# Performance work log

Hardware: AMD Instinct MI355X
Metric: run time of the kernel (lower is better)

The kernel has to match this reference:

```python
import jax, jax.numpy as jnp
import numpy as np

EPS = 1e-5
GROUPS = 32

def group_norm(x, w, b):
    B, C, D, H, W = x.shape
    g = x.reshape(B, GROUPS, C // GROUPS, D, H, W)
    mean = g.mean(axis=(2, 3, 4, 5), keepdims=True)
    var = g.var(axis=(2, 3, 4, 5), keepdims=True)
    g = (g - mean) * jax.lax.rsqrt(var + EPS)
    g = g.reshape(B, C, D, H, W)
    return g * w[None, :, None, None, None] + b[None, :, None, None, None]

def setup_inputs() -> dict:
    key = jax.random.key(0)
    ks = jax.random.split(key, 6)
    C = 256
    B, D, H, W = 2, 16, 16, 16
    xavier = math_scale = (6.0 / (C + C)) ** 0.5
    def xav(k):
        return jax.random.uniform(k, (C, C), jnp.float32, -xavier, xavier)
    return {
        "x": jax.random.normal(ks[0], (B, C, D, H, W), jnp.float32),
        "gn_w": jnp.ones((C,), jnp.float32),
        "gn_b": jnp.zeros((C,), jnp.float32),
        "wq": xav(ks[1]), "bq": jnp.zeros((C,), jnp.float32),
        "wk": xav(ks[2]), "bk": jnp.zeros((C,), jnp.float32),
        "wv": xav(ks[3]), "bv": jnp.zeros((C,), jnp.float32),
        "wp": xav(ks[4]), "bp": jnp.zeros((C,), jnp.float32),
    }

def reference(x, gn_w, gn_b, wq, bq, wk, bk, wv, bv, wp, bp):
    B, C, D, H, W = x.shape
    h = group_norm(x, gn_w, gn_b)
    hf = h.reshape(B, C, -1)  # (B, C, N)
    # 1x1x1 conv == channel-wise linear: weight (out_c, in_c)
    q = jnp.einsum('oc,bcn->bon', wq, hf) + bq[None, :, None]
    k = jnp.einsum('oc,bcn->bon', wk, hf) + bk[None, :, None]
    v = jnp.einsum('oc,bcn->bon', wv, hf) + bv[None, :, None]
    scale = C ** (-0.5)
    attn = jnp.einsum('bcn,bcm->bnm', q, k) * scale  # (B, N, N)
    attn = jax.nn.softmax(attn, axis=-1)
    out = jnp.einsum('bnm,bcm->bcn', attn, v)  # (B, C, N)
    out = jnp.einsum('oc,bcn->bon', wp, out) + bp[None, :, None]
    return x + out.reshape(B, C, D, H, W)
```

## Files before the change

### kernel.cpp

```cpp
#include <hip/hip_runtime.h>

#define C_DIM 256
#define N_SP  4096
#define B_DIM 2
#define CPG   8
#define EPS_GN 1e-5f
#define CN ((size_t)C_DIM * N_SP)

typedef unsigned short ushort_t;
typedef unsigned int uint_t;
typedef __attribute__((ext_vector_type(4))) float f32x4;
typedef __attribute__((ext_vector_type(16))) float f32x16;
typedef __attribute__((ext_vector_type(4))) unsigned int u32x4;
typedef __attribute__((ext_vector_type(8))) short bf16x8;

__device__ inline uint_t pkbf(float a, float b) {
  uint_t r;
  asm("v_cvt_pk_bf16_f32 %0, %1, %2" : "=v"(r) : "v"(a), "v"(b));
  return r;
}
__device__ inline float bf2f(uint_t u) {
  union { uint_t u; float f; } v; v.u = u << 16; return v.f;
}

#define GLOAD16(src, dst) __builtin_amdgcn_global_load_lds( \
    (const __attribute__((address_space(1))) unsigned int*)(src), \
    (__attribute__((address_space(3))) unsigned int*)(dst), 16, 0, 0)

__global__ __launch_bounds__(256) void wcvt_kernel(const float* __restrict__ wq,
    const float* __restrict__ wk, const float* __restrict__ wv,
    const float* __restrict__ wp, ushort_t* __restrict__ o) {
  int gid = blockIdx.x * 256 + threadIdx.x;
  int i4 = gid * 4;
  const float* s = (i4 < 65536) ? wq : (i4 < 131072) ? wk : (i4 < 196608) ? wv : wp;
  int off = i4 & 65535;
  float4 v = *(const float4*)(s + off);
  uint2 p; p.x = pkbf(v.x, v.y); p.y = pkbf(v.z, v.w);
  *(uint2*)&o[i4] = p;
}

__global__ __launch_bounds__(256) void gn_stats(const float* __restrict__ x,
    float* __restrict__ part) {
  const int bg = blockIdx.x, sub = blockIdx.y;
  const float* xp = x + (size_t)bg * CPG * N_SP + (size_t)sub * (CPG * N_SP / 4);
  const int tid = threadIdx.x;
  float s = 0.f, ss = 0.f;
  for (int i = tid; i < CPG * N_SP / 4; i += 256) {
    float v = xp[i];
    s += v; ss += v * v;
  }
#pragma unroll
  for (int off = 32; off > 0; off >>= 1) {
    s  += __shfl_down(s, off);
    ss += __shfl_down(ss, off);
  }
  __shared__ float rs[4], rss[4];
  const int wv = tid >> 6, ln = tid & 63;
  if (ln == 0) { rs[wv] = s; rss[wv] = ss; }
  __syncthreads();
  if (tid == 0) {
    part[(bg * 4 + sub) * 2]     = rs[0] + rs[1] + rs[2] + rs[3];
    part[(bg * 4 + sub) * 2 + 1] = rss[0] + rss[1] + rss[2] + rss[3];
  }
}

__global__ __launch_bounds__(256) void gn_apply(const float* __restrict__ x,
    const float* __restrict__ part, const float* __restrict__ w,
    const float* __restrict__ bgn, ushort_t* __restrict__ hT) {
  const int bg = blockIdx.x;
  const int b = bg >> 5, g = bg & 31;
  const int n0 = blockIdx.y * 256;
  const int tid = threadIdx.x;
  float S = 0.f, SS = 0.f;
#pragma unroll
  for (int i = 0; i < 4; ++i) {
    S  += part[(bg * 4 + i) * 2];
    SS += part[(bg * 4 + i) * 2 + 1];
  }
  const float mean = S / (float)(CPG * N_SP);
  const float var  = SS / (float)(CPG * N_SP) - mean * mean;
  const float rstd = rsqrtf(var + EPS_GN);
  float sc[8], sh[8];
#pragma unroll
  for (int c = 0; c < 8; ++c) {
    sc[c] = w[g * 8 + c] * rstd;
    sh[c] = bgn[g * 8 + c] - mean * sc[c];
  }
  __shared__ float tile[8][256];
  const float* xp = x + ((size_t)b * C_DIM + (size_t)g * CPG) * N_SP;
  for (int i = tid; i < 8 * 256; i += 256) {
    int cc = i >> 8, n = i & 255;
    tile[cc][n] = xp[(size_t)cc * N_SP + n0 + n];
  }
  __syncthreads();
  u32x4 pk4;
#pragma unroll
  for (int p = 0; p < 4; ++p)
    pk4[p] = pkbf(tile[2 * p][tid] * sc[2 * p] + sh[2 * p],
                  tile[2 * p + 1][tid] * sc[2 * p + 1] + sh[2 * p + 1]);
  *(u32x4*)&hT[((size_t)b * N_SP + n0 + tid) * C_DIM + g * 8] = pk4;
}

template <int MODE>
__global__ __launch_bounds__(256) void mgemm(
    const ushort_t* __restrict__ A, const ushort_t* __restrict__ Bm,
    const float* __restrict__ biasA, const float* __restrict__ biasB,
    ushort_t* __restrict__ outB, float* __restrict__ outF,
    const float* __restrict__ R, int aStride, int bStride, int ldo,
    size_t obStride) {
  __shared__ __align__(16) ushort_t a_lds[128 * 64];
  __shared__ __align__(16) ushort_t b_lds[128 * 64];
  const int bz = blockIdx.z;
  const ushort_t* Ab = A + (size_t)bz * aStride;
  const ushort_t* Bb = Bm + (size_t)bz * bStride;
  const int bm = blockIdx.y * 128, bn = blockIdx.x * 128;
  const int tid = threadIdx.x, wv = tid >> 6, ln = tid & 63;
  const int lo = ln & 15, g = ln >> 4;
  const int wr = wv >> 1, wc = wv & 1;

  f32x4 acc[4][4];
#pragma unroll
  for (int i = 0; i < 4; ++i)
#pragma unroll
    for (int j = 0; j < 4; ++j) acc[i][j] = (f32x4)(0.f);

  float bcol[4];
  float brow = 0.f;
  if (MODE == 0) {
#pragma unroll
    for (int ct = 0; ct < 4; ++ct) {
      int col = bn + wc * 64 + ct * 16 + lo;
      bcol[ct] = (col < 256) ? biasA[col] : biasB[col - 256];
    }
  } else {
    brow = biasA[bm + wr * 64 + ln];
  }

  for (int k0 = 0; k0 < C_DIM; k0 += 64) {
#pragma unroll
    for (int i = 0; i < 4; ++i) {
      int r0 = wv * 32 + i * 8;
      int row = r0 + (ln >> 3);
      GLOAD16(Ab + (size_t)(bm + row) * C_DIM + k0 + (((ln & 7) ^ (row & 7)) << 3),
              &a_lds[r0 * 64]);
      GLOAD16(Bb + (size_t)(bn + row) * C_DIM + k0 + (((ln & 7) ^ (row & 7)) << 3),
              &b_lds[r0 * 64]);
    }
    __syncthreads();
    bf16x8 af[4][2], bfr[4][2];
#pragma unroll
    for (int rt = 0; rt < 4; ++rt)
#pragma unroll
      for (int ks = 0; ks < 2; ++ks) {
        int row = wr * 64 + rt * 16 + lo;
        af[rt][ks] = *(const bf16x8*)&a_lds[row * 64 + (((ks * 4 + g) ^ (row & 7)) << 3)];
      }
#pragma unroll
    for (int ct = 0; ct < 4; ++ct)
#pragma unroll
      for (int ks = 0; ks < 2; ++ks) {
        int col = wc * 64 + ct * 16 + lo;
        bfr[ct][ks] = *(const bf16x8*)&b_lds[col * 64 + (((ks * 4 + g) ^ (col & 7)) << 3)];
      }
    __builtin_amdgcn_s_setprio(1);
#pragma unroll
    for (int ks = 0; ks < 2; ++ks)
#pragma unroll
      for (int rt = 0; rt < 4; ++rt)
#pragma unroll
        for (int ct = 0; ct < 4; ++ct)
          acc[rt][ct] = __builtin_amdgcn_mfma_f32_16x16x32_bf16(af[rt][ks], bfr[ct][ks], acc[rt][ct], 0, 0, 0);
    __builtin_amdgcn_s_setprio(0);
    __syncthreads();
  }

  float* wbase = (wv < 2 ? (float*)a_lds : (float*)b_lds) + (wv & 1) * 2048;
  const int grow = bm + wr * 64 + ln;
#pragma unroll
  for (int p = 0; p < 2; ++p) {
#pragma unroll
    for (int rt = 0; rt < 4; ++rt)
#pragma unroll
      for (int cth = 0; cth < 2; ++cth) {
        int ct = 2 * p + cth;
#pragma unroll
        for (int r = 0; r < 4; ++r) {
          int lrow = rt * 16 + 4 * g + r;
          int lcol = cth * 16 + lo;
          float v = acc[rt][ct][r];
          if (MODE == 0) v += bcol[ct];
          wbase[lrow * 32 + (lcol ^ ((lrow & 7) << 2))] = v;
        }
      }
    f32x4 buf[8];
#pragma unroll
    for (int cb = 0; cb < 8; ++cb) {
      int off = (4 * cb) ^ ((ln & 7) << 2);
      buf[cb] = *(const f32x4*)&wbase[ln * 32 + off];
    }
    const size_t obase = (size_t)grow * ldo + bn + wc * 64 + p * 32;
    if (MODE == 2) {
      const float* Rb = R + (size_t)bz * CN + obase;
      float* ob = outF + (size_t)bz * CN + obase;
#pragma unroll
      for (int cb = 0; cb < 8; ++cb) {
        f32x4 t = buf[cb];
        f32x4 rv = *(const f32x4*)&Rb[4 * cb];
#pragma unroll
        for (int j = 0; j < 4; ++j) t[j] += brow + rv[j];
        *(f32x4*)&ob[4 * cb] = t;
      }
    } else {
      float badd = (MODE == 0) ? 0.f : brow;
      ushort_t* ob = outB + (size_t)bz * obStride + obase;
      uint_t wpk[16];
#pragma unroll
      for (int k = 0; k < 16; ++k)
        wpk[k] = pkbf(buf[k >> 1][(k & 1) * 2] + badd, buf[k >> 1][(k & 1) * 2 + 1] + badd);
#pragma unroll
      for (int sidx = 0; sidx < 4; ++sidx) {
        u32x4 t;
        t[0] = wpk[4 * sidx]; t[1] = wpk[4 * sidx + 1];
        t[2] = wpk[4 * sidx + 2]; t[3] = wpk[4 * sidx + 3];
        *(u32x4*)&ob[sidx * 8] = t;
      }
    }
    __syncthreads();
  }
}

__device__ __forceinline__ void stage_kv(const ushort_t* __restrict__ ktb,
    const ushort_t* __restrict__ vtb, int k0, ushort_t* kbuf, ushort_t* vbuf,
    int wv, int ln) {
#pragma unroll
  for (int i = 0; i < 8; ++i) {
    int m = wv * 16 + i * 2 + (ln >> 5);
    int sl = ln & 31;
    GLOAD16(ktb + (size_t)(k0 + m) * 512 + ((sl ^ (m & 7)) * 8),
            kbuf + (wv * 16 + i * 2) * 256);
  }
#pragma unroll
  for (int i = 0; i < 8; ++i) {
    int c = wv * 64 + i * 8 + (ln >> 3);
    int sl = ln & 7;
    GLOAD16(vtb + (size_t)c * N_SP + k0 + ((sl ^ (c & 7)) * 8),
            vbuf + (wv * 64 + i * 8) * 64);
  }
}

__global__ __launch_bounds__(256, 1) void attn_mfma(
    const ushort_t* __restrict__ qk, const ushort_t* __restrict__ vt,
    ushort_t* __restrict__ pO, float* __restrict__ pml) {
  __shared__ __align__(16) ushort_t lds_all[32768 + 32768 + 9216];

  const int ksplit = blockIdx.y;
  const int b  = blockIdx.z;
  const int q0 = blockIdx.x * 128;
  const int tid = threadIdx.x;
  const int wv = tid >> 6;
  const int ln = tid & 63;
  const int lq = ln & 31;
  const int lh = ln >> 5;

  const ushort_t* qtb = qk + (size_t)b * N_SP * 512;
  const ushort_t* ktb = qtb + 256;
  const ushort_t* vtb = vt + (size_t)b * CN;
  ushort_t* p_base = lds_all + 65536 + wv * (32 * 72);

  bf16x8 qf[16];
  {
    const ushort_t* qp = qtb + (size_t)(q0 + wv * 32 + lq) * 512 + lh * 8;
#pragma unroll
    for (int ks = 0; ks < 16; ++ks) qf[ks] = *(const bf16x8*)(qp + ks * 16);
  }

  f32x16 oac[8];
#pragma unroll
  for (int i = 0; i < 8; ++i) oac[i] = (f32x16)(0.f);
  float m_run = -1e30f, l_run = 0.f;

  const int kbase = ksplit * 1024;
  stage_kv(ktb, vtb, kbase, lds_all, lds_all + 32768, wv, ln);
  __syncthreads();

  for (int t = 0; t < 16; ++t) {
    const int cur = t & 1;
    ushort_t* kb = lds_all + cur * 16384;
    ushort_t* vb = lds_all + 32768 + cur * 16384;
    if (t + 1 < 16)
      stage_kv(ktb, vtb, kbase + (t + 1) * 64,
               lds_all + (cur ^ 1) * 16384,
               lds_all + 32768 + (cur ^ 1) * 16384, wv, ln);

    f32x16 s0 = (f32x16)(0.f), s1 = (f32x16)(0.f);
    __builtin_amdgcn_s_setprio(1);
#pragma unroll
    for (int ks = 0; ks < 16; ++ks) {
      bf16x8 kf0 = *(const bf16x8*)&kb[(lq * 256 + ks * 16 + lh * 8) ^ ((lq & 7) << 3)];
      s0 = __builtin_amdgcn_mfma_f32_32x32x16_bf16(kf0, qf[ks], s0, 0, 0, 0);
      int m1 = 32 + lq;
      bf16x8 kf1 = *(const bf16x8*)&kb[(m1 * 256 + ks * 16 + lh * 8) ^ ((m1 & 7) << 3)];
      s1 = __builtin_amdgcn_mfma_f32_32x32x16_bf16(kf1, qf[ks], s1, 0, 0, 0);
    }
    __builtin_amdgcn_s_setprio(0);

    const float scale = 0.0625f;
    float mx[16];
#pragma unroll
    for (int r = 0; r < 16; ++r) mx[r] = fmaxf(s0[r], s1[r]);
#pragma unroll
    for (int r = 0; r < 8; ++r) mx[r] = fmaxf(mx[r], mx[r + 8]);
#pragma unroll
    for (int r = 0; r < 4; ++r) mx[r] = fmaxf(mx[r], mx[r + 4]);
    float pm = fmaxf(fmaxf(mx[0], mx[1]), fmaxf(mx[2], mx[3]));
    pm = fmaxf(pm, __shfl_xor(pm, 32));
    pm *= scale;
    float alpha = 1.f;
    if (!__all(pm <= m_run + 8.f)) {
      float mn = fmaxf(m_run, pm);
      alpha = __expf(m_run - mn);
      m_run = mn;
    }
    float rsum = 0.f;
#pragma unroll
    for (int g2 = 0; g2 < 4; ++g2) {
      float e00 = __expf(s0[4 * g2 + 0] * scale - m_run);
      float e01 = __expf(s0[4 * g2 + 1] * scale - m_run);
      float e02 = __expf(s0[4 * g2 + 2] * scale - m_run);
      float e03 = __expf(s0[4 * g2 + 3] * scale - m_run);
      float e10 = __expf(s1[4 * g2 + 0] * scale - m_run);
      float e11 = __expf(s1[4 * g2 + 1] * scale - m_run);
      float e12 = __expf(s1[4 * g2 + 2] * scale - m_run);
      float e13 = __expf(s1[4 * g2 + 3] * scale - m_run);
      rsum += ((e00 + e01) + (e02 + e03)) + ((e10 + e11) + (e12 + e13));
      uint2 wa; wa.x = pkbf(e00, e01); wa.y = pkbf(e02, e03);
      *(uint2*)&p_base[lq * 72 + 8 * g2 + 4 * lh] = wa;
      uint2 wb2; wb2.x = pkbf(e10, e11); wb2.y = pkbf(e12, e13);
      *(uint2*)&p_base[lq * 72 + 32 + 8 * g2 + 4 * lh] = wb2;
    }
    rsum += __shfl_xor(rsum, 32);
    l_run = l_run * alpha + rsum;
    if (!__all(alpha == 1.f)) {
#pragma unroll
      for (int i = 0; i < 8; ++i) oac[i] *= alpha;
    }

    __builtin_amdgcn_s_setprio(1);
#pragma unroll
    for (int ks2 = 0; ks2 < 4; ++ks2) {
      bf16x8 pf = *(const bf16x8*)&p_base[lq * 72 + ks2 * 16 + lh * 8];
#pragma unroll
      for (int ot = 0; ot < 8; ++ot) {
        int c = ot * 32 + lq;
        bf16x8 vf = *(const bf16x8*)&vb[(c * 64 + ks2 * 16 + lh * 8) ^ ((c & 7) << 3)];
        oac[ot] = __builtin_amdgcn_mfma_f32_32x32x16_bf16(vf, pf, oac[ot], 0, 0, 0);
      }
    }
    __builtin_amdgcn_s_setprio(0);
    __syncthreads();
  }

  float* sb = (float*)lds_all + wv * 8192;
#pragma unroll
  for (int ot = 0; ot < 8; ++ot)
#pragma unroll
    for (int r = 0; r < 16; ++r) {
      int cl = (r & 3) + 8 * (r >> 2) + 4 * lh;
      int c = ot * 32 + cl;
      sb[lq * 256 + (c ^ ((lq & 7) << 2))] = oac[ot][r];
    }
  {
    const int q = ln >> 1, half = ln & 1;
    const size_t row32 = (((size_t)(ksplit * B_DIM + b) * N_SP) + q0 + wv * 32 + q) * 128;
    uint_t* pO32 = (uint_t*)pO;
#pragma unroll
    for (int j = 0; j < 32; ++j) {
      f32x4 v4 = *(const f32x4*)&sb[q * 256 + ((half * 128 + 4 * j) ^ ((q & 7) << 2))];
      uint2 pk2; pk2.x = pkbf(v4[0], v4[1]); pk2.y = pkbf(v4[2], v4[3]);
      *(uint2*)&pO32[row32 + half * 64 + 2 * j] = pk2;
    }
  }
  if (ln < 32) {
    int qn = q0 + wv * 32 + lq;
    size_t mi = (((size_t)(ksplit * B_DIM + b) * N_SP) + qn) * 2;
    pml[mi] = m_run;
    pml[mi + 1] = l_run;
  }
}

__global__ __launch_bounds__(256) void merge_kernel(const ushort_t* __restrict__ pO,
    const float* __restrict__ pml, ushort_t* __restrict__ aoT) {
  const int b = blockIdx.y;
  const int n = blockIdx.x * 16 + (threadIdx.x >> 4);
  const int cg = threadIdx.x & 15;
  float mi[4], li[4];
#pragma unroll
  for (int i = 0; i < 4; ++i) {
    size_t o = (((size_t)(i * B_DIM + b) * N_SP) + n) * 2;
    mi[i] = pml[o]; li[i] = pml[o + 1];
  }
  float ms = fmaxf(fmaxf(mi[0], mi[1]), fmaxf(mi[2], mi[3]));
  float wsum = 0.f, wi[4];
#pragma unroll
  for (int i = 0; i < 4; ++i) { wi[i] = __expf(mi[i] - ms); wsum += wi[i] * li[i]; }
  float inv = 1.f / wsum;
  float acc[16] = {};
#pragma unroll
  for (int i = 0; i < 4; ++i) {
    const ushort_t* p = pO + (((size_t)(i * B_DIM + b) * N_SP) + n) * C_DIM + cg * 16;
    u32x4 a = *(const u32x4*)p;
    u32x4 c2 = *(const u32x4*)(p + 8);
#pragma unroll
    for (int j = 0; j < 4; ++j) {
      acc[2 * j]     += wi[i] * bf2f(a[j] & 0xffffu);
      acc[2 * j + 1] += wi[i] * bf2f(a[j] >> 16);
      acc[8 + 2 * j]     += wi[i] * bf2f(c2[j] & 0xffffu);
      acc[8 + 2 * j + 1] += wi[i] * bf2f(c2[j] >> 16);
    }
  }
  ushort_t* ob = aoT + ((size_t)b * N_SP + n) * C_DIM + cg * 16;
  u32x4 o0, o1;
#pragma unroll
  for (int k = 0; k < 4; ++k) o0[k] = pkbf(acc[2 * k] * inv, acc[2 * k + 1] * inv);
#pragma unroll
  for (int k = 0; k < 4; ++k) o1[k] = pkbf(acc[8 + 2 * k] * inv, acc[8 + 2 * k + 1] * inv);
  *(u32x4*)&ob[0] = o0;
  *(u32x4*)&ob[8] = o1;
}

extern "C" void kernel_launch(void* const* d_in, const int* in_sizes, int n_in,
                              void* d_out, int out_size, void* d_ws, size_t ws_size,
                              hipStream_t stream) {
  const float* x   = (const float*)d_in[0];
  const float* gnw = (const float*)d_in[1];
  const float* gnb = (const float*)d_in[2];
  const float* wq  = (const float*)d_in[3];
  const float* bq  = (const float*)d_in[4];
  const float* wk  = (const float*)d_in[5];
  const float* bk  = (const float*)d_in[6];
  const float* wv  = (const float*)d_in[7];
  const float* bv  = (const float*)d_in[8];
  const float* wp  = (const float*)d_in[9];
  const float* bp  = (const float*)d_in[10];
  float* out = (float*)d_out;

  char* w8 = (char*)d_ws;
  ushort_t* hT  = (ushort_t*)(w8);
  ushort_t* wb  = (ushort_t*)(w8 + (4u << 20));
  ushort_t* qkw = (ushort_t*)(w8 + (4u << 20) + (1u << 19));
  ushort_t* vN  = (ushort_t*)(w8 + (12u << 20) + (1u << 19));
  ushort_t* aoT = (ushort_t*)(w8 + (16u << 20) + (1u << 19));
  float*    pml = (float*)(w8 + (20u << 20) + (1u << 19));
  ushort_t* pO  = (ushort_t*)(w8 + (20u << 20) + (1u << 19) + (1u << 18));
  float*    gnp = (float*)(w8 + (36u << 20) + (1u << 19) + (1u << 18));

  ushort_t* wvb = wb + 131072;
  ushort_t* wpb = wb + 196608;

  wcvt_kernel<<<dim3(256), dim3(256), 0, stream>>>(wq, wk, wv, wp, wb);
  gn_stats<<<dim3(B_DIM * 32, 4), dim3(256), 0, stream>>>(x, gnp);
  gn_apply<<<dim3(B_DIM * 32, 16), dim3(256), 0, stream>>>(x, gnp, gnw, gnb, hT);

  mgemm<0><<<dim3(4, 32, B_DIM), dim3(256), 0, stream>>>(
      hT, wb, bq, bk, qkw, nullptr, nullptr, (int)CN, 0, 512, (size_t)N_SP * 512);
  mgemm<1><<<dim3(32, 2, B_DIM), dim3(256), 0, stream>>>(
      wvb, hT, bv, nullptr, vN, nullptr, nullptr, 0, (int)CN, N_SP, CN);

  attn_mfma<<<dim3(32, 4, B_DIM), dim3(256), 0, stream>>>(qkw, vN, pO, pml);
  merge_kernel<<<dim3(256, B_DIM), dim3(256), 0, stream>>>(pO, pml, aoT);

  mgemm<2><<<dim3(32, 2, B_DIM), dim3(256), 0, stream>>>(
      wpb, aoT, bp, nullptr, nullptr, out, x, 0, (int)CN, N_SP, CN);
}
```

Measured before the change: 118.1 us.

## Split attention KV range across two wave groups per block and merge in-block

The attention kernel now launches 512 threads: two groups of four waves each process half of the block's key range with their own single-buffered K/V tiles, then combine their softmax statistics and output accumulators through LDS before writing. The goal is more waves per CU, so MFMA work from one group can hide the other group's global-load latency. In exchange the cross-iteration double-buffer prefetch is gone, each tile now waits on a barrier before compute, and an extra reduction step is added. The P tile also moves from padded rows to an XOR-swizzled layout.

```diff
diff --git a/kernel.cpp b/kernel.cpp
--- a/kernel.cpp
+++ b/kernel.cpp
@@ -229,35 +229,18 @@
   }
 }
 
-__device__ __forceinline__ void stage_kv(const ushort_t* __restrict__ ktb,
-    const ushort_t* __restrict__ vtb, int k0, ushort_t* kbuf, ushort_t* vbuf,
-    int wv, int ln) {
-#pragma unroll
-  for (int i = 0; i < 8; ++i) {
-    int m = wv * 16 + i * 2 + (ln >> 5);
-    int sl = ln & 31;
-    GLOAD16(ktb + (size_t)(k0 + m) * 512 + ((sl ^ (m & 7)) * 8),
-            kbuf + (wv * 16 + i * 2) * 256);
-  }
-#pragma unroll
-  for (int i = 0; i < 8; ++i) {
-    int c = wv * 64 + i * 8 + (ln >> 3);
-    int sl = ln & 7;
-    GLOAD16(vtb + (size_t)c * N_SP + k0 + ((sl ^ (c & 7)) * 8),
-            vbuf + (wv * 64 + i * 8) * 64);
-  }
-}
-
-__global__ __launch_bounds__(256, 1) void attn_mfma(
+__global__ __launch_bounds__(512, 2) void attn_mfma(
     const ushort_t* __restrict__ qk, const ushort_t* __restrict__ vt,
     ushort_t* __restrict__ pO, float* __restrict__ pml) {
-  __shared__ __align__(16) ushort_t lds_all[32768 + 32768 + 9216];
+  __shared__ __align__(16) ushort_t lds_all[2][40960];
 
   const int ksplit = blockIdx.y;
   const int b  = blockIdx.z;
   const int q0 = blockIdx.x * 128;
   const int tid = threadIdx.x;
   const int wv = tid >> 6;
+  const int grp = wv >> 2;
+  const int wg  = wv & 3;
   const int ln = tid & 63;
   const int lq = ln & 31;
   const int lh = ln >> 5;
@@ -265,11 +248,14 @@
   const ushort_t* qtb = qk + (size_t)b * N_SP * 512;
   const ushort_t* ktb = qtb + 256;
   const ushort_t* vtb = vt + (size_t)b * CN;
-  ushort_t* p_base = lds_all + 65536 + wv * (32 * 72);
+
+  ushort_t* kb = &lds_all[grp][0];
+  ushort_t* vb = &lds_all[grp][16384];
+  ushort_t* p_base = &lds_all[grp][32768 + wg * 2048];
 
   bf16x8 qf[16];
   {
-    const ushort_t* qp = qtb + (size_t)(q0 + wv * 32 + lq) * 512 + lh * 8;
+    const ushort_t* qp = qtb + (size_t)(q0 + wg * 32 + lq) * 512 + lh * 8;
 #pragma unroll
     for (int ks = 0; ks < 16; ++ks) qf[ks] = *(const bf16x8*)(qp + ks * 16);
   }
@@ -279,18 +265,24 @@
   for (int i = 0; i < 8; ++i) oac[i] = (f32x16)(0.f);
   float m_run = -1e30f, l_run = 0.f;
 
-  const int kbase = ksplit * 1024;
-  stage_kv(ktb, vtb, kbase, lds_all, lds_all + 32768, wv, ln);
-  __syncthreads();
-
-  for (int t = 0; t < 16; ++t) {
-    const int cur = t & 1;
-    ushort_t* kb = lds_all + cur * 16384;
-    ushort_t* vb = lds_all + 32768 + cur * 16384;
-    if (t + 1 < 16)
-      stage_kv(ktb, vtb, kbase + (t + 1) * 64,
-               lds_all + (cur ^ 1) * 16384,
-               lds_all + 32768 + (cur ^ 1) * 16384, wv, ln);
+  const int kgbase = ksplit * 1024 + grp * 512;
+  for (int t = 0; t < 8; ++t) {
+    const int k0 = kgbase + t * 64;
+#pragma unroll
+    for (int i = 0; i < 8; ++i) {
+      int r0 = wg * 16 + i * 2;
+      int m = r0 + (ln >> 5);
+      GLOAD16(ktb + (size_t)(k0 + m) * 512 + (((ln & 31) ^ (m & 7)) * 8),
+              kb + r0 * 256);
+    }
+#pragma unroll
+    for (int i = 0; i < 8; ++i) {
+      int c0 = wg * 64 + i * 8;
+      int c = c0 + (ln >> 3);
+      GLOAD16(vtb + (size_t)c * N_SP + k0 + (((ln & 7) ^ (c & 7)) * 8),
+              vb + c0 * 64);
+    }
+    __syncthreads();
 
     f32x16 s0 = (f32x16)(0.f), s1 = (f32x16)(0.f);
     __builtin_amdgcn_s_setprio(1);
@@ -334,9 +326,9 @@
       float e13 = __expf(s1[4 * g2 + 3] * scale - m_run);
       rsum += ((e00 + e01) + (e02 + e03)) + ((e10 + e11) + (e12 + e13));
       uint2 wa; wa.x = pkbf(e00, e01); wa.y = pkbf(e02, e03);
-      *(uint2*)&p_base[lq * 72 + 8 * g2 + 4 * lh] = wa;
+      *(uint2*)&p_base[lq * 64 + ((8 * g2 + 4 * lh) ^ ((lq & 7) << 3))] = wa;
       uint2 wb2; wb2.x = pkbf(e10, e11); wb2.y = pkbf(e12, e13);
-      *(uint2*)&p_base[lq * 72 + 32 + 8 * g2 + 4 * lh] = wb2;
+      *(uint2*)&p_base[lq * 64 + ((32 + 8 * g2 + 4 * lh) ^ ((lq & 7) << 3))] = wb2;
     }
     rsum += __shfl_xor(rsum, 32);
     l_run = l_run * alpha + rsum;
@@ -348,7 +340,7 @@
     __builtin_amdgcn_s_setprio(1);
 #pragma unroll
     for (int ks2 = 0; ks2 < 4; ++ks2) {
-      bf16x8 pf = *(const bf16x8*)&p_base[lq * 72 + ks2 * 16 + lh * 8];
+      bf16x8 pf = *(const bf16x8*)&p_base[lq * 64 + ((ks2 * 16 + lh * 8) ^ ((lq & 7) << 3))];
 #pragma unroll
       for (int ot = 0; ot < 8; ++ot) {
         int c = ot * 32 + lq;
@@ -360,31 +352,61 @@
     __syncthreads();
   }
 
-  float* sb = (float*)lds_all + wv * 8192;
-#pragma unroll
-  for (int ot = 0; ot < 8; ++ot)
-#pragma unroll
-    for (int r = 0; r < 16; ++r) {
-      int cl = (r & 3) + 8 * (r >> 2) + 4 * lh;
-      int c = ot * 32 + cl;
-      sb[lq * 256 + (c ^ ((lq & 7) << 2))] = oac[ot][r];
-    }
+  float* mlx = (float*)&lds_all[1][32768];
+  if (lh == 0) {
+    int idx = (((grp * 4 + wg) * 32) + lq) * 2;
+    mlx[idx] = m_run;
+    mlx[idx + 1] = l_run;
+  }
+  __syncthreads();
+  float a_self, l_fin, m_fin;
   {
-    const int q = ln >> 1, half = ln & 1;
-    const size_t row32 = (((size_t)(ksplit * B_DIM + b) * N_SP) + q0 + wv * 32 + q) * 128;
-    uint_t* pO32 = (uint_t*)pO;
-#pragma unroll
-    for (int j = 0; j < 32; ++j) {
-      f32x4 v4 = *(const f32x4*)&sb[q * 256 + ((half * 128 + 4 * j) ^ ((q & 7) << 2))];
-      uint2 pk2; pk2.x = pkbf(v4[0], v4[1]); pk2.y = pkbf(v4[2], v4[3]);
-      *(uint2*)&pO32[row32 + half * 64 + 2 * j] = pk2;
-    }
-  }
-  if (ln < 32) {
-    int qn = q0 + wv * 32 + lq;
+    int idx = ((((grp ^ 1) * 4 + wg) * 32) + lq) * 2;
+    float mo = mlx[idx];
+    float lo_ = mlx[idx + 1];
+    m_fin = fmaxf(m_run, mo);
+    a_self = __expf(m_run - m_fin);
+    l_fin = l_run * a_self + lo_ * __expf(mo - m_fin);
+  }
+#pragma unroll
+  for (int i = 0; i < 8; ++i) oac[i] *= a_self;
+  if (grp == 0 && lh == 0) {
+    int qn = q0 + wg * 32 + lq;
     size_t mi = (((size_t)(ksplit * B_DIM + b) * N_SP) + qn) * 2;
-    pml[mi] = m_run;
-    pml[mi + 1] = l_run;
+    pml[mi] = m_fin;
+    pml[mi + 1] = l_fin;
+  }
+  __syncthreads();
+
+  float* sbA = (float*)&lds_all[0][0] + wg * 4096;
+  float* sbB = (float*)&lds_all[1][0] + wg * 4096;
+  float* mysb = grp ? sbB : sbA;
+  uint_t* pO32 = (uint_t*)pO;
+  const size_t rowbase = (((size_t)(ksplit * B_DIM + b) * N_SP) + q0 + wg * 32) * 128;
+#pragma unroll
+  for (int p = 0; p < 2; ++p) {
+#pragma unroll
+    for (int ot = 0; ot < 4; ++ot)
+#pragma unroll
+      for (int r = 0; r < 16; ++r) {
+        int cl = (r & 3) + 8 * (r >> 2) + 4 * lh;
+        int c_loc = ot * 32 + cl;
+        mysb[lq * 128 + (c_loc ^ ((lq & 7) << 2))] = oac[p * 4 + ot][r];
+      }
+    __syncthreads();
+    if (grp == 0) {
+      const int q = ln >> 1, half = ln & 1;
+#pragma unroll
+      for (int j = 0; j < 16; ++j) {
+        int off = (half * 64 + 4 * j) ^ ((q & 7) << 2);
+        f32x4 va = *(const f32x4*)&sbA[q * 128 + off];
+        f32x4 vb4 = *(const f32x4*)&sbB[q * 128 + off];
+        f32x4 sum = va + vb4;
+        uint2 pk2; pk2.x = pkbf(sum[0], sum[1]); pk2.y = pkbf(sum[2], sum[3]);
+        *(uint2*)&pO32[rowbase + (size_t)q * 128 + p * 64 + half * 32 + 2 * j] = pk2;
+      }
+    }
+    __syncthreads();
   }
 }
 
@@ -466,7 +488,7 @@
   mgemm<1><<<dim3(32, 2, B_DIM), dim3(256), 0, stream>>>(
       wvb, hT, bv, nullptr, vN, nullptr, nullptr, 0, (int)CN, N_SP, CN);
 
-  attn_mfma<<<dim3(32, 4, B_DIM), dim3(256), 0, stream>>>(qkw, vN, pO, pml);
+  attn_mfma<<<dim3(32, 4, B_DIM), dim3(512), 0, stream>>>(qkw, vN, pO, pml);
   merge_kernel<<<dim3(256, B_DIM), dim3(256), 0, stream>>>(pO, pml, aoT);
 
   mgemm<2><<<dim3(32, 2, B_DIM), dim3(256), 0, stream>>>(
```

Result: slower. 296.7 us (+151.3%).
